# Performance work log

Hardware: AMD Instinct MI355X
Metric: run time of the kernel (lower is better)

Reference implementation:

```python
import jax, jax.numpy as jnp
import numpy as np

N, I, D, K = 64, 8192, 128, 16


def setup_inputs() -> dict:
    key = jax.random.key(0)
    k1, k2 = jax.random.split(key)
    x = jax.random.normal(k1, (N, I, D), dtype=jnp.float32)
    # each point belongs to one of k clusters of its own batch element -> offset n*K
    ci = jax.random.randint(k2, (N, I), 0, K) + jnp.arange(N)[:, None] * K
    return {
        "feature_matrix_batch": x,
        "cluster_index": ci.reshape(-1).astype(jnp.int32),  # [N*I]
        "k": K,
    }


def reference(feature_matrix_batch, cluster_index, k):
    n, i, d = feature_matrix_batch.shape
    flat = feature_matrix_batch.reshape(-1, d)  # [N*I, D]
    # scatter_max over segment ids -> [N*k, D]
    out = jax.ops.segment_max(flat, cluster_index, num_segments=n * k)
    return out.reshape(n, k, d)
```

## Files before the change

kernel.cpp:

```cpp
#include <hip/hip_runtime.h>
#include <stdint.h>

#define NB 64
#define NI 8192
#define ND 128
#define NK 16
#define SEG (NK * ND)
#define OUT_ELEMS (NB * SEG)
#define MAPPED_NEG_INF 0x007FFFFFu

#define PPB_A 512
#define BPB_A (NI / PPB_A)
#define GRID_A (NB * BPB_A)
#define WS_NEEDED ((size_t)GRID_A * SEG * 4)

#define PPB_B 256
#define BPB_B (NI / PPB_B)

__device__ __forceinline__ uint32_t map_f32(float f) {
    uint32_t b = __float_as_uint(f);
    return b ^ ((uint32_t)((int32_t)b >> 31) | 0x80000000u);
}
__device__ __forceinline__ uint32_t unmap_u32(uint32_t m) {
    return (m & 0x80000000u) ? (m ^ 0x80000000u) : ~m;
}

__global__ __launch_bounds__(256, 4) void seg_partial(
        const float* __restrict__ x,
        const int* __restrict__ ci,
        uint32_t* __restrict__ ws) {
    __shared__ uint32_t loc[SEG];
    __shared__ int cidx[PPB_A];

    const int t = threadIdx.x;
    const int b = blockIdx.x;
    const int batch = b >> 4;
    const int chunk = (b & (BPB_A - 1)) * PPB_A;
    const int row0 = batch * NI + chunk;

    for (int i = t; i < SEG; i += 256) loc[i] = MAPPED_NEG_INF;
    for (int i = t; i < PPB_A; i += 256) cidx[i] = ci[row0 + i] - batch * NK;
    __syncthreads();

    const int lane32 = t & 31;
    const int rsub = t >> 5;
    const float4* xrow = (const float4*)(x + (size_t)row0 * ND) + lane32;

    #pragma unroll 2
    for (int it = 0; it < PPB_A / 8; ++it) {
        const int i = it * 8 + rsub;
        const int c = cidx[i];
        float4 v = xrow[(size_t)i * (ND / 4)];
        uint32_t* lp = &loc[(c << 7) + lane32];
        atomicMax(&lp[0],  map_f32(v.x));
        atomicMax(&lp[32], map_f32(v.y));
        atomicMax(&lp[64], map_f32(v.z));
        atomicMax(&lp[96], map_f32(v.w));
    }
    __syncthreads();

    uint32_t* wb = ws + (size_t)b * SEG;
    for (int o = t; o < SEG; o += 256) {
        const int c = o >> 7;
        const int d = o & 127;
        wb[o] = loc[(c << 7) + ((d & 3) << 5) + (d >> 2)];
    }
}

__global__ __launch_bounds__(256) void seg_reduce(
        const uint32_t* __restrict__ ws,
        uint32_t* __restrict__ out) {
    const int idx = blockIdx.x * 256 + threadIdx.x;
    const int batch = idx >> 11;
    const int o = idx & (SEG - 1);
    const uint32_t* p = ws + (size_t)batch * BPB_A * SEG + o;
    uint32_t m = MAPPED_NEG_INF;
    #pragma unroll
    for (int j = 0; j < BPB_A; ++j) m = max(m, p[(size_t)j * SEG]);
    out[idx] = unmap_u32(m);
}

__global__ __launch_bounds__(256) void seg_init(uint32_t* __restrict__ out) {
    int idx = blockIdx.x * 256 + threadIdx.x;
    out[idx] = MAPPED_NEG_INF;
}

__global__ __launch_bounds__(256, 8) void seg_max_kernel(
        const float* __restrict__ x,
        const int* __restrict__ ci,
        uint32_t* __restrict__ out) {
    __shared__ uint32_t loc[SEG];
    __shared__ int cidx[PPB_B];

    const int t = threadIdx.x;
    const int b = blockIdx.x;
    const int batch = b >> 5;
    const int chunk = (b & (BPB_B - 1)) * PPB_B;
    const int row0 = batch * NI + chunk;

    for (int i = t; i < SEG; i += 256) loc[i] = MAPPED_NEG_INF;
    cidx[t] = ci[row0 + t] - batch * NK;
    __syncthreads();

    const int lane32 = t & 31;
    const int rsub = t >> 5;
    const float4* xrow = (const float4*)(x + (size_t)row0 * ND) + lane32;

    for (int it = 0; it < PPB_B / 8; ++it) {
        const int i = it * 8 + rsub;
        const int c = cidx[i];
        float4 v = xrow[(size_t)i * (ND / 4)];
        uint32_t* lp = &loc[(c << 7) + lane32];
        atomicMax(&lp[0],  map_f32(v.x));
        atomicMax(&lp[32], map_f32(v.y));
        atomicMax(&lp[64], map_f32(v.z));
        atomicMax(&lp[96], map_f32(v.w));
    }
    __syncthreads();

    uint32_t* ob = out + (size_t)batch * SEG;
    for (int o = t; o < SEG; o += 256) {
        const int c = o >> 7;
        const int d = o & 127;
        uint32_t v = loc[(c << 7) + ((d & 3) << 5) + (d >> 2)];
        if (v != MAPPED_NEG_INF) atomicMax(&ob[o], v);
    }
}

__global__ __launch_bounds__(256) void seg_decode(uint32_t* __restrict__ out) {
    int idx = blockIdx.x * 256 + threadIdx.x;
    out[idx] = unmap_u32(out[idx]);
}

extern "C" void kernel_launch(void* const* d_in, const int* in_sizes, int n_in,
                              void* d_out, int out_size, void* d_ws, size_t ws_size,
                              hipStream_t stream) {
    const float* x = (const float*)d_in[0];
    const int* ci = (const int*)d_in[1];
    uint32_t* out = (uint32_t*)d_out;

    if (ws_size >= WS_NEEDED) {
        uint32_t* ws = (uint32_t*)d_ws;
        seg_partial<<<GRID_A, 256, 0, stream>>>(x, ci, ws);
        seg_reduce<<<OUT_ELEMS / 256, 256, 0, stream>>>(ws, out);
    } else {
        seg_init<<<OUT_ELEMS / 256, 256, 0, stream>>>(out);
        seg_max_kernel<<<NB * BPB_B, 256, 0, stream>>>(x, ci, out);
        seg_decode<<<OUT_ELEMS / 256, 256, 0, stream>>>(out);
    }
}
```

Before: 52.95 us.

## Template partial-reduce kernels, use finer chunks, vectorize reduce and index loads

Templates the partial kernel on points-per-block and, when the workspace allows, launches 2048 blocks of 256 points each with an 8-wave occupancy hint, up from 1024 blocks of 512. The reduce kernel now handles four outputs per thread with vector loads, and cluster indices are loaded as int4. Feature loads use nontemporal hints. The aim is more parallelism and latency hiding in the partial pass and wider memory access in the reduce. The cost is twice the workspace traffic, since 32 partials per batch must be written and read back instead of 16.

```diff
diff --git a/kernel.cpp b/kernel.cpp
--- a/kernel.cpp
+++ b/kernel.cpp
@@ -9,13 +9,8 @@
 #define OUT_ELEMS (NB * SEG)
 #define MAPPED_NEG_INF 0x007FFFFFu
 
-#define PPB_A 512
-#define BPB_A (NI / PPB_A)
-#define GRID_A (NB * BPB_A)
-#define WS_NEEDED ((size_t)GRID_A * SEG * 4)
-
-#define PPB_B 256
-#define BPB_B (NI / PPB_B)
+typedef float f4 __attribute__((ext_vector_type(4)));
+typedef uint32_t u4 __attribute__((ext_vector_type(4)));
 
 __device__ __forceinline__ uint32_t map_f32(float f) {
     uint32_t b = __float_as_uint(f);
@@ -25,32 +20,38 @@
     return (m & 0x80000000u) ? (m ^ 0x80000000u) : ~m;
 }
 
-__global__ __launch_bounds__(256, 4) void seg_partial(
+template <int PPB>
+__global__ __launch_bounds__(256, 8) void seg_partial(
         const float* __restrict__ x,
         const int* __restrict__ ci,
         uint32_t* __restrict__ ws) {
+    constexpr int BPB = NI / PPB;
     __shared__ uint32_t loc[SEG];
-    __shared__ int cidx[PPB_A];
+    __shared__ int cidx[PPB];
 
     const int t = threadIdx.x;
     const int b = blockIdx.x;
-    const int batch = b >> 4;
-    const int chunk = (b & (BPB_A - 1)) * PPB_A;
-    const int row0 = batch * NI + chunk;
+    const int batch = b / BPB;
+    const int row0 = batch * NI + (b % BPB) * PPB;
 
     for (int i = t; i < SEG; i += 256) loc[i] = MAPPED_NEG_INF;
-    for (int i = t; i < PPB_A; i += 256) cidx[i] = ci[row0 + i] - batch * NK;
+    if (t < PPB / 4) {
+        int4 c = ((const int4*)(ci + row0))[t];
+        const int base = batch * NK;
+        c.x -= base; c.y -= base; c.z -= base; c.w -= base;
+        ((int4*)cidx)[t] = c;
+    }
     __syncthreads();
 
     const int lane32 = t & 31;
     const int rsub = t >> 5;
-    const float4* xrow = (const float4*)(x + (size_t)row0 * ND) + lane32;
+    const f4* xrow = (const f4*)(x + (size_t)row0 * ND) + lane32;
 
     #pragma unroll 2
-    for (int it = 0; it < PPB_A / 8; ++it) {
+    for (int it = 0; it < PPB / 8; ++it) {
         const int i = it * 8 + rsub;
         const int c = cidx[i];
-        float4 v = xrow[(size_t)i * (ND / 4)];
+        f4 v = __builtin_nontemporal_load(&xrow[(size_t)i * (ND / 4)]);
         uint32_t* lp = &loc[(c << 7) + lane32];
         atomicMax(&lp[0],  map_f32(v.x));
         atomicMax(&lp[32], map_f32(v.y));
@@ -67,18 +68,32 @@
     }
 }
 
+template <int BPB>
 __global__ __launch_bounds__(256) void seg_reduce(
         const uint32_t* __restrict__ ws,
         uint32_t* __restrict__ out) {
     const int idx = blockIdx.x * 256 + threadIdx.x;
-    const int batch = idx >> 11;
-    const int o = idx & (SEG - 1);
-    const uint32_t* p = ws + (size_t)batch * BPB_A * SEG + o;
-    uint32_t m = MAPPED_NEG_INF;
+    const int batch = idx >> 9;
+    const int o4 = idx & (SEG / 4 - 1);
+    const u4* p = (const u4*)(ws + (size_t)batch * BPB * SEG) + o4;
+    u4 m;
+    m.x = m.y = m.z = m.w = MAPPED_NEG_INF;
     #pragma unroll
-    for (int j = 0; j < BPB_A; ++j) m = max(m, p[(size_t)j * SEG]);
-    out[idx] = unmap_u32(m);
+    for (int j = 0; j < BPB; ++j) {
+        u4 v = p[(size_t)j * (SEG / 4)];
+        m.x = v.x > m.x ? v.x : m.x;
+        m.y = v.y > m.y ? v.y : m.y;
+        m.z = v.z > m.z ? v.z : m.z;
+        m.w = v.w > m.w ? v.w : m.w;
+    }
+    u4 r;
+    r.x = unmap_u32(m.x); r.y = unmap_u32(m.y);
+    r.z = unmap_u32(m.z); r.w = unmap_u32(m.w);
+    ((u4*)out)[idx] = r;
 }
+
+#define PPB_B 256
+#define BPB_B (NI / PPB_B)
 
 __global__ __launch_bounds__(256) void seg_init(uint32_t* __restrict__ out) {
     int idx = blockIdx.x * 256 + threadIdx.x;
@@ -95,8 +110,7 @@
     const int t = threadIdx.x;
     const int b = blockIdx.x;
     const int batch = b >> 5;
-    const int chunk = (b & (BPB_B - 1)) * PPB_B;
-    const int row0 = batch * NI + chunk;
+    const int row0 = batch * NI + (b & (BPB_B - 1)) * PPB_B;
 
     for (int i = t; i < SEG; i += 256) loc[i] = MAPPED_NEG_INF;
     cidx[t] = ci[row0 + t] - batch * NK;
@@ -104,12 +118,12 @@
 
     const int lane32 = t & 31;
     const int rsub = t >> 5;
-    const float4* xrow = (const float4*)(x + (size_t)row0 * ND) + lane32;
+    const f4* xrow = (const f4*)(x + (size_t)row0 * ND) + lane32;
 
     for (int it = 0; it < PPB_B / 8; ++it) {
         const int i = it * 8 + rsub;
         const int c = cidx[i];
-        float4 v = xrow[(size_t)i * (ND / 4)];
+        f4 v = xrow[(size_t)i * (ND / 4)];
         uint32_t* lp = &loc[(c << 7) + lane32];
         atomicMax(&lp[0],  map_f32(v.x));
         atomicMax(&lp[32], map_f32(v.y));
@@ -139,10 +153,17 @@
     const int* ci = (const int*)d_in[1];
     uint32_t* out = (uint32_t*)d_out;
 
-    if (ws_size >= WS_NEEDED) {
+    const size_t ws_16mb = (size_t)2048 * SEG * 4;
+    const size_t ws_8mb  = (size_t)1024 * SEG * 4;
+
+    if (ws_size >= ws_16mb) {
         uint32_t* ws = (uint32_t*)d_ws;
-        seg_partial<<<GRID_A, 256, 0, stream>>>(x, ci, ws);
-        seg_reduce<<<OUT_ELEMS / 256, 256, 0, stream>>>(ws, out);
+        seg_partial<256><<<2048, 256, 0, stream>>>(x, ci, ws);
+        seg_reduce<32><<<OUT_ELEMS / 4 / 256, 256, 0, stream>>>(ws, out);
+    } else if (ws_size >= ws_8mb) {
+        uint32_t* ws = (uint32_t*)d_ws;
+        seg_partial<512><<<1024, 256, 0, stream>>>(x, ci, ws);
+        seg_reduce<16><<<OUT_ELEMS / 4 / 256, 256, 0, stream>>>(ws, out);
     } else {
         seg_init<<<OUT_ELEMS / 256, 256, 0, stream>>>(out);
         seg_max_kernel<<<NB * BPB_B, 256, 0, stream>>>(x, ci, out);
```

New measurement: 55.27 us. +4.4%, slower.
